# Optimization experiments

Measured on AMD Instinct MI355X. Metric: run time of the kernel, lower is better.

## Reference

```python
import jax, jax.numpy as jnp
import numpy as np

N = 50000      # nodes
E = 800000     # edges (before self-loops)
IN = 256       # input_dim
HID = 72       # hidden_dim
HEADS = 4
NEG_SLOPE = 0.2  # PyG GATConv default leaky-relu slope


def setup_inputs() -> dict:
    key = jax.random.key(0)
    ks = jax.random.split(key, 16)
    rn = lambda k, shape: jax.random.normal(k, shape, jnp.float32) * 0.05
    return {
        "x": jax.random.normal(ks[0], (N, IN), jnp.float32),
        "edge_index": jax.random.randint(ks[1], (2, E), 0, N),
        "W_in": rn(ks[2], (IN, HID)), "b_in": jnp.zeros((HID,), jnp.float32),
        "W1": rn(ks[3], (HID, HEADS * HID)),
        "a_src1": rn(ks[4], (HEADS, HID)), "a_dst1": rn(ks[5], (HEADS, HID)),
        "b1": jnp.zeros((HEADS * HID,), jnp.float32),
        "W2": rn(ks[6], (HEADS * HID, HID)),
        "a_src2": rn(ks[7], (1, HID)), "a_dst2": rn(ks[8], (1, HID)),
        "b2": jnp.zeros((HID,), jnp.float32),
        "W3": rn(ks[9], (HID, HID)),
        "a_src3": rn(ks[10], (1, HID)), "a_dst3": rn(ks[11], (1, HID)),
        "b3": jnp.zeros((HID,), jnp.float32),
        "Ws1": rn(ks[12], (HID, 32)), "bs1": jnp.zeros((32,), jnp.float32),
        "Ws2": rn(ks[13], (32, 1)), "bs2": jnp.zeros((1,), jnp.float32),
    }


def gat_conv(x, src, dst, W, a_src, a_dst, bias, concat):
    # PyG GATConv (eval mode): per-head linear, leaky-relu attention logits,
    # segment softmax over incoming edges per destination, scatter-aggregate.
    H, C = a_src.shape
    h = (x @ W).reshape(-1, H, C)                      # [N, H, C]
    logit_s = jnp.einsum('nhc,hc->nh', h, a_src)       # [N, H]
    logit_d = jnp.einsum('nhc,hc->nh', h, a_dst)       # [N, H]
    e = jax.nn.leaky_relu(logit_s[src] + logit_d[dst], NEG_SLOPE)   # [Et, H]
    emax = jax.ops.segment_max(e, dst, num_segments=N)
    emax = jnp.where(jnp.isfinite(emax), emax, 0.0)
    p = jnp.exp(e - emax[dst])
    denom = jax.ops.segment_sum(p, dst, num_segments=N)
    alpha = p / jnp.maximum(denom[dst], 1e-16)         # [Et, H]
    out = jax.ops.segment_sum(h[src] * alpha[:, :, None], dst, num_segments=N)
    out = out.reshape(-1, H * C) if concat else out.mean(axis=1)
    return out + bias


def reference(x, edge_index, W_in, b_in,
              W1, a_src1, a_dst1, b1,
              W2, a_src2, a_dst2, b2,
              W3, a_src3, a_dst3, b3,
              Ws1, bs1, Ws2, bs2):
    loops = jnp.arange(N)                              # PyG add_self_loops=True
    src = jnp.concatenate([edge_index[0], loops])
    dst = jnp.concatenate([edge_index[1], loops])
    x0 = x @ W_in + b_in                               # [N, HID]
    h = jax.nn.elu(gat_conv(x0, src, dst, W1, a_src1, a_dst1, b1, True))
    h = jax.nn.elu(gat_conv(h, src, dst, W2, a_src2, a_dst2, b2, False))
    h = jax.nn.elu(gat_conv(h, src, dst, W3, a_src3, a_dst3, b3, False))
    h = h + x0
    score = jax.nn.relu(h @ Ws1 + bs1) @ Ws2 + bs2     # dropout = identity (eval)
    return score.squeeze(-1)                           # [N]
```

## Files before the change

### kernel.cpp

```cpp
#include <hip/hip_runtime.h>
#include <hip/hip_fp16.h>
#include <cmath>

#define NN 50000
#define EE 800000
#define ET (EE + NN)
#define IN_DIM 256
#define HID 72
#define CAP 96

typedef __attribute__((ext_vector_type(8))) short s8v;
typedef __attribute__((ext_vector_type(4))) short s4v;
typedef __attribute__((ext_vector_type(4))) float f4v;
typedef __attribute__((ext_vector_type(2))) float f2v;

__device__ __forceinline__ ushort f2bf(float x) {
    uint u = __float_as_uint(x);
    return (ushort)((u + 0x7fffu + ((u >> 16) & 1u)) >> 16);
}
__device__ __forceinline__ float bf2f(ushort h) {
    return __uint_as_float(((uint)h) << 16);
}
__device__ __forceinline__ void split4(const float4& v, s4v& h, s4v& l) {
    ushort h0 = f2bf(v.x), h1 = f2bf(v.y), h2 = f2bf(v.z), h3 = f2bf(v.w);
    h = (s4v){(short)h0, (short)h1, (short)h2, (short)h3};
    l = (s4v){(short)f2bf(v.x - bf2f(h0)), (short)f2bf(v.y - bf2f(h1)),
              (short)f2bf(v.z - bf2f(h2)), (short)f2bf(v.w - bf2f(h3))};
}
__device__ __forceinline__ f4v mfma16(s8v a, s8v b, f4v c) {
    return __builtin_amdgcn_mfma_f32_16x16x32_bf16(a, b, c, 0, 0, 0);
}
__device__ __forceinline__ f2v unpack_h2(uint pv) {
    __half2 hv = __builtin_bit_cast(__half2, pv);
    return (f2v){__low2float(hv), __high2float(hv)};
}
__device__ __forceinline__ uint pack_h2(float a, float b) {
    __half2 hp = __floats2half2_rn(a, b);
    return __builtin_bit_cast(uint, hp);
}
__device__ __forceinline__ f2v fma2(float w, f2v c, f2v a) {
    return __builtin_elementwise_fma((f2v){w, w}, c, a);
}

__global__ void adj_kernel(const int* __restrict__ ei, int* __restrict__ deg,
                           int* __restrict__ ell) {
    int i = blockIdx.x * blockDim.x + threadIdx.x;
    if (i >= ET) return;
    int src = (i < EE) ? ei[i] : (i - EE);
    int dst = (i < EE) ? ei[EE + i] : (i - EE);
    int pos = atomicAdd(&deg[dst], 1);
    if (pos < CAP) ell[dst * CAP + pos] = src;
}

__device__ __forceinline__ void wsplit_one(const float* W, int ldw, int K,
        int idx, short* outH, short* outL) {
    int h = idx / (72 * K);
    int rem = idx - h * 72 * K;
    int n = rem / K, k = rem - n * K;
    float v = W[(size_t)k * ldw + h * 72 + n];
    ushort hi = f2bf(v);
    outH[idx] = (short)hi;
    outL[idx] = (short)f2bf(v - bf2f(hi));
}

#define PR0 18432
#define PR1 (PR0 + 20736)
#define PR2 (PR1 + 20736)
#define PR3 (PR2 + 5184)
#define PRTOT (PR3 + 288)

__global__ __launch_bounds__(256) void prep_kernel(
        const float* __restrict__ W_in, const float* __restrict__ W1,
        const float* __restrict__ W2, const float* __restrict__ W3,
        const float* __restrict__ a_src, const float* __restrict__ a_dst,
        short* __restrict__ BtInH, short* __restrict__ BtInL,
        short* __restrict__ Bt1H, short* __restrict__ Bt1L,
        short* __restrict__ Bt2H, short* __restrict__ Bt2L,
        short* __restrict__ Bt3H, short* __restrict__ Bt3L,
        float* __restrict__ wsrc, float* __restrict__ wdst) {
    int gid = blockIdx.x * 256 + threadIdx.x;
    if (gid < PR0) {
        wsplit_one(W_in, 72, 256, gid, BtInH, BtInL);
    } else if (gid < PR1) {
        wsplit_one(W1, 288, 72, gid - PR0, Bt1H, Bt1L);
    } else if (gid < PR2) {
        wsplit_one(W2, 72, 288, gid - PR1, Bt2H, Bt2L);
    } else if (gid < PR3) {
        wsplit_one(W3, 72, 72, gid - PR2, Bt3H, Bt3L);
    } else if (gid < PRTOT) {
        int j = gid - PR3;
        int h = j / HID, k = j % HID;
        const float* wrow = W1 + (size_t)k * (4 * HID) + h * HID;
        const float* as = a_src + h * HID;
        const float* ad = a_dst + h * HID;
        float s = 0.f, d = 0.f;
        for (int c = 0; c < HID; ++c) {
            float w = wrow[c];
            s = fmaf(w, as[c], s);
            d = fmaf(w, ad[c], d);
        }
        wsrc[j] = s;
        wdst[j] = d;
    }
}

template <int NLOGIT, bool ELU_EPI, bool BATCHED, bool PACKOUT, bool APACK>
__global__ __launch_bounds__(256) void gemm_mfma(
        const void* __restrict__ Ain, const short* __restrict__ BtH,
        const short* __restrict__ BtL, const float* __restrict__ bias,
        float* __restrict__ C, uint* __restrict__ Cp, int ldp,
        const float* __restrict__ lvs, const float* __restrict__ lvd,
        float* __restrict__ ls, float* __restrict__ ld,
        int M, int K, int lda, int Nfull) {
    __shared__ __align__(16) short AhS[64 * 40], AlS[64 * 40];
    __shared__ __align__(16) short BhS[80 * 40], BlS[80 * 40];

    int tid = threadIdx.x;
    int row0 = blockIdx.x * 64;
    int hh = BATCHED ? blockIdx.y : 0;
    int aoff = BATCHED ? hh * (APACK ? 36 : 72) : 0;
    int coff = BATCHED ? hh * 72 : 0;
    const short* bhg = BtH + (size_t)hh * 72 * K;
    const short* blg = BtL + (size_t)hh * 72 * K;

    for (int i = tid; i < 8 * 40; i += 256) {
        BhS[72 * 40 + i] = 0;
        BlS[72 * 40 + i] = 0;
    }

    int w = tid >> 6;
    int lane = tid & 63;
    int q = lane >> 4, l16 = lane & 15;

    f4v acc[5];
    #pragma unroll
    for (int f = 0; f < 5; ++f) acc[f] = (f4v)0.f;

    int ar = tid >> 2;
    int aseg = tid & 3;
    bool arok = (row0 + ar) < M;
    const float* aptrf = nullptr;
    const uint*  aptru = nullptr;
    if constexpr (APACK) {
        aptru = (const uint*)Ain + (size_t)(row0 + ar) * lda + aoff;
    } else {
        aptrf = (const float*)Ain + (size_t)(row0 + ar) * lda + aoff;
    }
    int bn0 = tid >> 2, bq0 = tid & 3;
    int bn1 = (tid + 256) >> 2;

    float4 va, vb;
    s8v bh0, bl0, bh1, bl1;
    auto gload = [&](int k0) {
        va = (float4){0, 0, 0, 0};
        vb = (float4){0, 0, 0, 0};
        int ka = k0 + aseg * 8;
        if constexpr (APACK) {
            if (arok && ka < K) {
                uint4 u = *(const uint4*)(aptru + (ka >> 1));
                f2v p0 = unpack_h2(u.x), p1 = unpack_h2(u.y);
                f2v p2 = unpack_h2(u.z), p3 = unpack_h2(u.w);
                va = (float4){p0.x, p0.y, p1.x, p1.y};
                vb = (float4){p2.x, p2.y, p3.x, p3.y};
            }
        } else {
            if (arok && ka < K)     va = *(const float4*)(aptrf + ka);
            if (arok && ka + 4 < K) vb = *(const float4*)(aptrf + ka + 4);
        }
        bh0 = (s8v)0; bl0 = (s8v)0;
        int kb = k0 + bq0 * 8;
        if (kb < K) {
            bh0 = *(const s8v*)(bhg + (size_t)bn0 * K + kb);
            bl0 = *(const s8v*)(blg + (size_t)bn0 * K + kb);
        }
        bh1 = (s8v)0; bl1 = (s8v)0;
        if (tid < 32 && kb < K) {
            bh1 = *(const s8v*)(bhg + (size_t)bn1 * K + kb);
            bl1 = *(const s8v*)(blg + (size_t)bn1 * K + kb);
        }
    };
    auto commit = [&]() {
        s4v h0, l0, h1, l1;
        split4(va, h0, l0);
        split4(vb, h1, l1);
        *(s4v*)&AhS[ar * 40 + aseg * 8]     = h0;
        *(s4v*)&AhS[ar * 40 + aseg * 8 + 4] = h1;
        *(s4v*)&AlS[ar * 40 + aseg * 8]     = l0;
        *(s4v*)&AlS[ar * 40 + aseg * 8 + 4] = l1;
        *(s8v*)&BhS[bn0 * 40 + bq0 * 8] = bh0;
        *(s8v*)&BlS[bn0 * 40 + bq0 * 8] = bl0;
        if (tid < 32) {
            *(s8v*)&BhS[bn1 * 40 + bq0 * 8] = bh1;
            *(s8v*)&BlS[bn1 * 40 + bq0 * 8] = bl1;
        }
    };

    int ntiles = (K + 31) / 32;
    gload(0);
    for (int t = 0; t < ntiles; ++t) {
        commit();
        __syncthreads();
        if (t + 1 < ntiles) gload((t + 1) * 32);
        s8v ah = *(const s8v*)&AhS[(w * 16 + l16) * 40 + q * 8];
        s8v al = *(const s8v*)&AlS[(w * 16 + l16) * 40 + q * 8];
        #pragma unroll
        for (int f = 0; f < 5; ++f) {
            s8v bh = *(const s8v*)&BhS[(f * 16 + l16) * 40 + q * 8];
            s8v bl = *(const s8v*)&BlS[(f * 16 + l16) * 40 + q * 8];
            acc[f] = mfma16(ah, bh, acc[f]);
            acc[f] = mfma16(ah, bl, acc[f]);
            acc[f] = mfma16(al, bh, acc[f]);
        }
        __syncthreads();
    }

    float v[5][4];
    #pragma unroll
    for (int f = 0; f < 5; ++f) {
        int col = f * 16 + l16;
        bool cv = col < 72;
        #pragma unroll
        for (int r = 0; r < 4; ++r) {
            float t = acc[f][r];
            if (cv && bias) t += bias[coff + col];
            if (ELU_EPI) t = (t > 0.f) ? t : expm1f(t);
            v[f][r] = cv ? t : 0.f;
        }
    }
    if (NLOGIT > 0) {
        #pragma unroll
        for (int h2 = 0; h2 < NLOGIT; ++h2) {
            #pragma unroll
            for (int r = 0; r < 4; ++r) {
                float s = 0.f, d = 0.f;
                #pragma unroll
                for (int f = 0; f < 5; ++f) {
                    int col = f * 16 + l16;
                    float lw = (col < 72) ? lvs[h2 * 72 + col] : 0.f;
                    float dw = (col < 72) ? lvd[h2 * 72 + col] : 0.f;
                    s = fmaf(v[f][r], lw, s);
                    d = fmaf(v[f][r], dw, d);
                }
                s += __shfl_xor(s, 1); s += __shfl_xor(s, 2);
                s += __shfl_xor(s, 4); s += __shfl_xor(s, 8);
                d += __shfl_xor(d, 1); d += __shfl_xor(d, 2);
                d += __shfl_xor(d, 4); d += __shfl_xor(d, 8);
                int gr = row0 + w * 16 + q * 4 + r;
                if (l16 == 0 && gr < M) {
                    ls[gr * NLOGIT + h2] = s;
                    ld[gr * NLOGIT + h2] = d;
                }
            }
        }
    }
    if (PACKOUT) {
        #pragma unroll
        for (int f = 0; f < 5; ++f) {
            int col = f * 16 + l16;
            #pragma unroll
            for (int r = 0; r < 4; ++r) {
                float vo = __shfl_xor(v[f][r], 1);
                if ((l16 & 1) == 0 && col < 72) {
                    int gr = row0 + w * 16 + q * 4 + r;
                    if (gr < M) {
                        Cp[(size_t)gr * ldp + ((coff + col) >> 1)] =
                            pack_h2(v[f][r], vo);
                    }
                }
            }
        }
    }
    if (C != nullptr) {
        #pragma unroll
        for (int f = 0; f < 5; ++f) {
            int col = f * 16 + l16;
            if (col >= 72) continue;
            #pragma unroll
            for (int r = 0; r < 4; ++r) {
                int gr = row0 + w * 16 + q * 4 + r;
                if (gr < M) C[(size_t)gr * Nfull + coff + col] = v[f][r];
            }
        }
    }
}

template <int H, bool EPI, bool ADD_RES, bool POUT>
__global__ __launch_bounds__(64) void agg_gather(
        const uint* __restrict__ featp,
        const float* __restrict__ ls, const float* __restrict__ ld,
        const int* __restrict__ degv, const int* __restrict__ ell,
        const float* __restrict__ bias, const float* __restrict__ res,
        float* __restrict__ out, uint* __restrict__ outp, int n) {
    __shared__ float wsh[64 * H];
    __shared__ int ssh[64];
    int wid = blockIdx.x;
    int lane = threadIdx.x;
    int deg = min(degv[wid], CAP);
    const int* row = ell + (size_t)wid * CAP;

    float ldh[H];
    if (H == 4) {
        float4 t = ((const float4*)ld)[wid];
        ldh[0] = t.x; ldh[1] = t.y; ldh[2] = t.z; ldh[3] = t.w;
    } else {
        ldh[0] = ld[wid];
    }

    f2v acc2[H];
    #pragma unroll
    for (int h = 0; h < H; ++h) acc2[h] = (f2v)0.f;

    if (deg <= 64) {
        bool act = lane < deg;
        int s = row[act ? lane : 0];
        ssh[lane] = s;
        float e[H];
        float ev[H];
        if (H == 4) {
            float4 lv = ((const float4*)ls)[s];
            ev[0] = lv.x; ev[1] = lv.y; ev[2] = lv.z; ev[3] = lv.w;
        } else {
            ev[0] = ls[s];
        }
        #pragma unroll
        for (int h = 0; h < H; ++h) {
            float vv = ev[h] + ldh[h];
            vv = (vv > 0.f) ? vv : 0.2f * vv;
            e[h] = act ? vv : -__builtin_inff();
        }
        float wv[H];
        #pragma unroll
        for (int h = 0; h < H; ++h) {
            float mh = e[h];
            #pragma unroll
            for (int off = 32; off; off >>= 1) mh = fmaxf(mh, __shfl_xor(mh, off));
            float ph = act ? expf(e[h] - mh) : 0.f;
            float sh = ph;
            #pragma unroll
            for (int off = 32; off; off >>= 1) sh += __shfl_xor(sh, off);
            wv[h] = ph / fmaxf(sh, 1e-16f);
        }
        if (H == 4) {
            ((float4*)wsh)[lane] = (float4){wv[0], wv[1], wv[2], wv[3]};
        } else {
            wsh[lane] = wv[0];
        }
        __syncthreads();

        int nb = (deg + 7) & ~7;
        const uint* rowbase = featp + (lane < 36 ? lane : 0);
        for (int t = 0; t < nb; t += 8) {
            int si[8];
            #pragma unroll
            for (int u = 0; u < 8; ++u) si[u] = ssh[t + u];
            uint pv[8];
            #pragma unroll
            for (int u = 0; u < 8; ++u) pv[u] = rowbase[(size_t)si[u] * 36];
            #pragma unroll
            for (int u = 0; u < 8; ++u) {
                f2v c2 = unpack_h2(pv[u]);
                if constexpr (H == 4) {
                    float4 we = ((const float4*)wsh)[t + u];
                    acc2[0] = fma2(we.x, c2, acc2[0]);
                    acc2[1] = fma2(we.y, c2, acc2[1]);
                    acc2[2] = fma2(we.z, c2, acc2[2]);
                    acc2[3] = fma2(we.w, c2, acc2[3]);
                } else {
                    acc2[0] = fma2(wsh[t + u], c2, acc2[0]);
                }
            }
        }
    } else {
        float m[H];
        #pragma unroll
        for (int h = 0; h < H; ++h) m[h] = -__builtin_inff();
        for (int i = lane; i < deg; i += 64) {
            int s = row[i];
            float e[H];
            if (H == 4) {
                float4 lv = ((const float4*)ls)[s];
                e[0] = lv.x; e[1] = lv.y; e[2] = lv.z; e[3] = lv.w;
            } else {
                e[0] = ls[s];
            }
            #pragma unroll
            for (int h = 0; h < H; ++h) {
                float vv = e[h] + ldh[h];
                vv = (vv > 0.f) ? vv : 0.2f * vv;
                m[h] = fmaxf(m[h], vv);
            }
        }
        #pragma unroll
        for (int h = 0; h < H; ++h)
            #pragma unroll
            for (int off = 32; off; off >>= 1) m[h] = fmaxf(m[h], __shfl_xor(m[h], off));

        float ssum[H];
        #pragma unroll
        for (int h = 0; h < H; ++h) ssum[h] = 0.f;
        for (int i = lane; i < deg; i += 64) {
            int s = row[i];
            float e[H];
            if (H == 4) {
                float4 lv = ((const float4*)ls)[s];
                e[0] = lv.x; e[1] = lv.y; e[2] = lv.z; e[3] = lv.w;
            } else {
                e[0] = ls[s];
            }
            #pragma unroll
            for (int h = 0; h < H; ++h) {
                float vv = e[h] + ldh[h];
                vv = (vv > 0.f) ? vv : 0.2f * vv;
                ssum[h] += expf(vv - m[h]);
            }
        }
        #pragma unroll
        for (int h = 0; h < H; ++h)
            #pragma unroll
            for (int off = 32; off; off >>= 1) ssum[h] += __shfl_xor(ssum[h], off);
        float inv[H];
        #pragma unroll
        for (int h = 0; h < H; ++h) inv[h] = 1.f / fmaxf(ssum[h], 1e-16f);

        for (int base = 0; base < deg; base += 64) {
            int i = base + lane;
            int lim = min(64, deg - base);
            if (i < deg) {
                int s = row[i];
                ssh[lane] = s;
                float e[H];
                if (H == 4) {
                    float4 lv = ((const float4*)ls)[s];
                    e[0] = lv.x; e[1] = lv.y; e[2] = lv.z; e[3] = lv.w;
                } else {
                    e[0] = ls[s];
                }
                if (H == 4) {
                    float p0 = expf(((e[0] + ldh[0] > 0.f) ? e[0] + ldh[0] : 0.2f * (e[0] + ldh[0])) - m[0]) * inv[0];
                    float p1 = expf(((e[1] + ldh[1] > 0.f) ? e[1] + ldh[1] : 0.2f * (e[1] + ldh[1])) - m[1]) * inv[1];
                    float p2 = expf(((e[2] + ldh[2] > 0.f) ? e[2] + ldh[2] : 0.2f * (e[2] + ldh[2])) - m[2]) * inv[2];
                    float p3 = expf(((e[3] + ldh[3] > 0.f) ? e[3] + ldh[3] : 0.2f * (e[3] + ldh[3])) - m[3]) * inv[3];
                    ((float4*)wsh)[lane] = (float4){p0, p1, p2, p3};
                } else {
                    float vv = e[0] + ldh[0];
                    vv = (vv > 0.f) ? vv : 0.2f * vv;
                    wsh[lane] = expf(vv - m[0]) * inv[0];
                }
            }
            __syncthreads();
            for (int t = 0; t < lim; ++t) {
                uint pv = featp[(size_t)ssh[t] * 36 + (lane < 36 ? lane : 0)];
                f2v c2 = unpack_h2(pv);
                if constexpr (H == 4) {
                    float4 we = ((const float4*)wsh)[t];
                    acc2[0] = fma2(we.x, c2, acc2[0]);
                    acc2[1] = fma2(we.y, c2, acc2[1]);
                    acc2[2] = fma2(we.z, c2, acc2[2]);
                    acc2[3] = fma2(we.w, c2, acc2[3]);
                } else {
                    acc2[0] = fma2(wsh[t], c2, acc2[0]);
                }
            }
            __syncthreads();
        }
    }

    if (lane < 36) {
        #pragma unroll
        for (int h = 0; h < H; ++h) {
            float v0 = acc2[h].x, v1 = acc2[h].y;
            if (EPI) {
                v0 += bias[2 * lane];
                v1 += bias[2 * lane + 1];
                v0 = (v0 > 0.f) ? v0 : expm1f(v0);
                v1 = (v1 > 0.f) ? v1 : expm1f(v1);
                if (ADD_RES) {
                    float2 rr = *(const float2*)&res[(size_t)wid * HID + 2 * lane];
                    v0 += rr.x; v1 += rr.y;
                }
            }
            if (POUT) {
                outp[(size_t)wid * (H * 36) + h * 36 + lane] = pack_h2(v0, v1);
            } else {
                *(float2*)&out[(size_t)wid * (H * HID) + h * HID + 2 * lane] =
                    (float2){v0, v1};
            }
        }
    }
}

__global__ __launch_bounds__(256) void score_kernel(
        const float* __restrict__ h, const float* __restrict__ Ws1, const float* __restrict__ bs1,
        const float* __restrict__ Ws2, const float* __restrict__ bs2,
        float* __restrict__ out, int n) {
    int sub = threadIdx.x >> 5;
    int j = threadIdx.x & 31;
    int node = blockIdx.x * 8 + sub;
    if (node >= n) return;
    const float* row = h + (size_t)node * HID;
    float acc = bs1[j];
    #pragma unroll 8
    for (int c = 0; c < HID; ++c) acc = fmaf(row[c], Ws1[c * 32 + j], acc);
    float v = fmaxf(acc, 0.f) * Ws2[j];
    #pragma unroll
    for (int off = 16; off; off >>= 1) v += __shfl_down(v, off, 32);
    if (j == 0) out[node] = v + bs2[0];
}

extern "C" void kernel_launch(void* const* d_in, const int* in_sizes, int n_in,
                              void* d_out, int out_size, void* d_ws, size_t ws_size,
                              hipStream_t stream) {
    const float* x      = (const float*)d_in[0];
    const int*   ei     = (const int*)  d_in[1];
    const float* W_in   = (const float*)d_in[2];
    const float* b_in   = (const float*)d_in[3];
    const float* W1     = (const float*)d_in[4];
    const float* a_src1 = (const float*)d_in[5];
    const float* a_dst1 = (const float*)d_in[6];
    const float* b1     = (const float*)d_in[7];
    const float* W2     = (const float*)d_in[8];
    const float* a_src2 = (const float*)d_in[9];
    const float* a_dst2 = (const float*)d_in[10];
    const float* b2     = (const float*)d_in[11];
    const float* W3     = (const float*)d_in[12];
    const float* a_src3 = (const float*)d_in[13];
    const float* a_dst3 = (const float*)d_in[14];
    const float* b3     = (const float*)d_in[15];
    const float* Ws1    = (const float*)d_in[16];
    const float* bs1    = (const float*)d_in[17];
    const float* Ws2    = (const float*)d_in[18];
    const float* bs2    = (const float*)d_in[19];
    float* out = (float*)d_out;

    float* ws    = (float*)d_ws;
    float* x0    = ws;
    float* h3    = x0 + (size_t)NN * HID;
    float* ls    = h3 + (size_t)NN * HID;
    float* ld    = ls + (size_t)NN * 4;
    float* wsrc1 = ld + (size_t)NN * 4;
    float* wdst1 = wsrc1 + 288;
    int* deg    = (int*)(wdst1 + 288);
    int* ell    = deg + NN;
    uintptr_t bp = ((uintptr_t)(ell + (size_t)NN * CAP) + 15) & ~(uintptr_t)15;
    short* BtInH = (short*)bp;
    short* BtInL = BtInH + 18432;
    short* Bt1H  = BtInL + 18432;
    short* Bt1L  = Bt1H + 20736;
    short* Bt2H  = Bt1L + 20736;
    short* Bt2L  = Bt2H + 20736;
    short* Bt3H  = Bt2L + 20736;
    short* Bt3L  = Bt3H + 5184;
    uint*  x0p   = (uint*)(Bt3L + 5184);
    uint*  a1p   = x0p + (size_t)NN * 36;
    uint*  h1p   = a1p + (size_t)NN * 144;
    uint*  hp2p  = h1p + (size_t)NN * 144;
    uint*  h2p   = hp2p + (size_t)NN * 36;
    uint*  hp3p  = h2p + (size_t)NN * 36;

    hipMemsetAsync(deg, 0, NN * sizeof(int), stream);

    const int egrid = (ET + 255) / 256;
    adj_kernel<<<egrid, 256, 0, stream>>>(ei, deg, ell);

    prep_kernel<<<(PRTOT + 255) / 256, 256, 0, stream>>>(
        W_in, W1, W2, W3, a_src1, a_dst1,
        BtInH, BtInL, Bt1H, Bt1L, Bt2H, Bt2L, Bt3H, Bt3L, wsrc1, wdst1);

    const int mblocks = (NN + 63) / 64;
    gemm_mfma<4, false, false, true, false><<<dim3(mblocks, 1), 256, 0, stream>>>(
        x, BtInH, BtInL, b_in, x0, x0p, 36, wsrc1, wdst1, ls, ld,
        NN, IN_DIM, IN_DIM, HID);
    agg_gather<4, false, false, true><<<NN, 64, 0, stream>>>(
        x0p, ls, ld, deg, ell, nullptr, nullptr, nullptr, a1p, NN);
    gemm_mfma<0, true, true, true, true><<<dim3(mblocks, 4), 256, 0, stream>>>(
        a1p, Bt1H, Bt1L, b1, nullptr, h1p, 144, nullptr, nullptr, nullptr, nullptr,
        NN, HID, 144, 0);
    gemm_mfma<1, false, false, true, true><<<dim3(mblocks, 1), 256, 0, stream>>>(
        h1p, Bt2H, Bt2L, nullptr, nullptr, hp2p, 36, a_src2, a_dst2, ls, ld,
        NN, 288, 144, 0);
    agg_gather<1, true, false, true><<<NN, 64, 0, stream>>>(
        hp2p, ls, ld, deg, ell, b2, nullptr, nullptr, h2p, NN);
    gemm_mfma<1, false, false, true, true><<<dim3(mblocks, 1), 256, 0, stream>>>(
        h2p, Bt3H, Bt3L, nullptr, nullptr, hp3p, 36, a_src3, a_dst3, ls, ld,
        NN, HID, 36, 0);
    agg_gather<1, true, true, false><<<NN, 64, 0, stream>>>(
        hp3p, ls, ld, deg, ell, b3, x0, h3, nullptr, NN);
    score_kernel<<<(NN + 7) / 8, 256, 0, stream>>>(h3, Ws1, bs1, Ws2, bs2, out, NN);
}
```

Before: 398.4 us.

## Fuse adjacency build into first GEMM launch and store ELL indices as ushort

Removes the separate adjacency kernel and adds extra blocks to the first GEMM launch that build the degree counts and ELL neighbor lists, so the atomic scatter runs alongside the input projection. Each adjacency thread now processes four edges through vectorized int4 loads. Neighbor indices are stored as 16-bit values, halving ELL memory traffic in the three gather kernels. Storing indices as ushort truncates node ids above 65535, which is safe only because N is 50000.

Result: faster. 372.7 us (-6.5%).

```diff
diff --git a/kernel.cpp b/kernel.cpp
--- a/kernel.cpp
+++ b/kernel.cpp
@@ -40,16 +40,6 @@
 }
 __device__ __forceinline__ f2v fma2(float w, f2v c, f2v a) {
     return __builtin_elementwise_fma((f2v){w, w}, c, a);
-}
-
-__global__ void adj_kernel(const int* __restrict__ ei, int* __restrict__ deg,
-                           int* __restrict__ ell) {
-    int i = blockIdx.x * blockDim.x + threadIdx.x;
-    if (i >= ET) return;
-    int src = (i < EE) ? ei[i] : (i - EE);
-    int dst = (i < EE) ? ei[EE + i] : (i - EE);
-    int pos = atomicAdd(&deg[dst], 1);
-    if (pos < CAP) ell[dst * CAP + pos] = src;
 }
 
 __device__ __forceinline__ void wsplit_one(const float* W, int ldw, int K,
@@ -104,18 +94,51 @@
     }
 }
 
-template <int NLOGIT, bool ELU_EPI, bool BATCHED, bool PACKOUT, bool APACK>
+template <int NLOGIT, bool ELU_EPI, bool BATCHED, bool PACKOUT, bool APACK, bool ADJ>
 __global__ __launch_bounds__(256) void gemm_mfma(
         const void* __restrict__ Ain, const short* __restrict__ BtH,
         const short* __restrict__ BtL, const float* __restrict__ bias,
         float* __restrict__ C, uint* __restrict__ Cp, int ldp,
         const float* __restrict__ lvs, const float* __restrict__ lvd,
         float* __restrict__ ls, float* __restrict__ ld,
-        int M, int K, int lda, int Nfull) {
+        int M, int K, int lda, int Nfull,
+        const int* __restrict__ eiw, int* __restrict__ degw,
+        ushort* __restrict__ ellw, int gemmBlocks) {
     __shared__ __align__(16) short AhS[64 * 40], AlS[64 * 40];
     __shared__ __align__(16) short BhS[80 * 40], BlS[80 * 40];
 
     int tid = threadIdx.x;
+
+    if (ADJ && (int)blockIdx.x >= gemmBlocks) {
+        int t = (blockIdx.x - gemmBlocks) * 256 + tid;
+        int i0 = t * 4;
+        if (i0 < ET) {
+            if (i0 + 3 < EE) {
+                int4 s4 = *(const int4*)(eiw + i0);
+                int4 d4 = *(const int4*)(eiw + EE + i0);
+                int ss[4] = {s4.x, s4.y, s4.z, s4.w};
+                int dd[4] = {d4.x, d4.y, d4.z, d4.w};
+                #pragma unroll
+                for (int u = 0; u < 4; ++u) {
+                    int pos = atomicAdd(&degw[dd[u]], 1);
+                    if (pos < CAP) ellw[dd[u] * CAP + pos] = (ushort)ss[u];
+                }
+            } else {
+                #pragma unroll
+                for (int u = 0; u < 4; ++u) {
+                    int i = i0 + u;
+                    if (i < ET) {
+                        int src = (i < EE) ? eiw[i] : (i - EE);
+                        int dst = (i < EE) ? eiw[EE + i] : (i - EE);
+                        int pos = atomicAdd(&degw[dst], 1);
+                        if (pos < CAP) ellw[dst * CAP + pos] = (ushort)src;
+                    }
+                }
+            }
+        }
+        return;
+    }
+
     int row0 = blockIdx.x * 64;
     int hh = BATCHED ? blockIdx.y : 0;
     int aoff = BATCHED ? hh * (APACK ? 36 : 72) : 0;
@@ -288,7 +311,7 @@
 __global__ __launch_bounds__(64) void agg_gather(
         const uint* __restrict__ featp,
         const float* __restrict__ ls, const float* __restrict__ ld,
-        const int* __restrict__ degv, const int* __restrict__ ell,
+        const int* __restrict__ degv, const ushort* __restrict__ ell,
         const float* __restrict__ bias, const float* __restrict__ res,
         float* __restrict__ out, uint* __restrict__ outp, int n) {
     __shared__ float wsh[64 * H];
@@ -296,7 +319,7 @@
     int wid = blockIdx.x;
     int lane = threadIdx.x;
     int deg = min(degv[wid], CAP);
-    const int* row = ell + (size_t)wid * CAP;
+    const ushort* row = ell + (size_t)wid * CAP;
 
     float ldh[H];
     if (H == 4) {
@@ -539,8 +562,8 @@
     float* ld    = ls + (size_t)NN * 4;
     float* wsrc1 = ld + (size_t)NN * 4;
     float* wdst1 = wsrc1 + 288;
-    int* deg    = (int*)(wdst1 + 288);
-    int* ell    = deg + NN;
+    int* deg     = (int*)(wdst1 + 288);
+    ushort* ell  = (ushort*)(deg + NN);
     uintptr_t bp = ((uintptr_t)(ell + (size_t)NN * CAP) + 15) & ~(uintptr_t)15;
     short* BtInH = (short*)bp;
     short* BtInL = BtInH + 18432;
@@ -559,30 +582,29 @@
 
     hipMemsetAsync(deg, 0, NN * sizeof(int), stream);
 
-    const int egrid = (ET + 255) / 256;
-    adj_kernel<<<egrid, 256, 0, stream>>>(ei, deg, ell);
-
     prep_kernel<<<(PRTOT + 255) / 256, 256, 0, stream>>>(
         W_in, W1, W2, W3, a_src1, a_dst1,
         BtInH, BtInL, Bt1H, Bt1L, Bt2H, Bt2L, Bt3H, Bt3L, wsrc1, wdst1);
 
     const int mblocks = (NN + 63) / 64;
-    gemm_mfma<4, false, false, true, false><<<dim3(mblocks, 1), 256, 0, stream>>>(
+    const int adjBlocks = (ET / 4 + 255) / 256;
+    gemm_mfma<4, false, false, true, false, true>
+        <<<dim3(mblocks + adjBlocks, 1), 256, 0, stream>>>(
         x, BtInH, BtInL, b_in, x0, x0p, 36, wsrc1, wdst1, ls, ld,
-        NN, IN_DIM, IN_DIM, HID);
+        NN, IN_DIM, IN_DIM, HID, ei, deg, ell, mblocks);
     agg_gather<4, false, false, true><<<NN, 64, 0, stream>>>(
         x0p, ls, ld, deg, ell, nullptr, nullptr, nullptr, a1p, NN);
-    gemm_mfma<0, true, true, true, true><<<dim3(mblocks, 4), 256, 0, stream>>>(
+    gemm_mfma<0, true, true, true, true, false><<<dim3(mblocks, 4), 256, 0, stream>>>(
         a1p, Bt1H, Bt1L, b1, nullptr, h1p, 144, nullptr, nullptr, nullptr, nullptr,
-        NN, HID, 144, 0);
-    gemm_mfma<1, false, false, true, true><<<dim3(mblocks, 1), 256, 0, stream>>>(
+        NN, HID, 144, 0, nullptr, nullptr, nullptr, 0);
+    gemm_mfma<1, false, false, true, true, false><<<dim3(mblocks, 1), 256, 0, stream>>>(
         h1p, Bt2H, Bt2L, nullptr, nullptr, hp2p, 36, a_src2, a_dst2, ls, ld,
-        NN, 288, 144, 0);
+        NN, 288, 144, 0, nullptr, nullptr, nullptr, 0);
     agg_gather<1, true, false, true><<<NN, 64, 0, stream>>>(
         hp2p, ls, ld, deg, ell, b2, nullptr, nullptr, h2p, NN);
-    gemm_mfma<1, false, false, true, true><<<dim3(mblocks, 1), 256, 0, stream>>>(
+    gemm_mfma<1, false, false, true, true, false><<<dim3(mblocks, 1), 256, 0, stream>>>(
         h2p, Bt3H, Bt3L, nullptr, nullptr, hp3p, 36, a_src3, a_dst3, ls, ld,
-        NN, HID, 36, 0);
+        NN, HID, 36, 0, nullptr, nullptr, nullptr, 0);
     agg_gather<1, true, true, false><<<NN, 64, 0, stream>>>(
         hp3p, ls, ld, deg, ell, b3, x0, h3, nullptr, NN);
     score_kernel<<<(NN + 7) / 8, 256, 0, stream>>>(h3, Ws1, bs1, Ws2, bs2, out, NN);
```
